# Performance work log

Hardware: AMD Instinct MI355X
Metric: run time of the kernel (lower is better)

## Reference

```python
import jax, jax.numpy as jnp
import numpy as np

V, E, H = 50000, 200, 256
B, R, S, W = 16, 16, 16, 32


def gru_last(x, Wih, Whh, bih, bhh):
    """PyTorch-style GRU, return final hidden state.
    x: [N, T, D]; Wih: [3H, D]; Whh: [3H, H]. Gate order: r, z, n."""
    gx = jnp.einsum('ntd,gd->ntg', x, Wih) + bih  # precompute input gates [N,T,3H]
    h0 = jnp.zeros((x.shape[0], Whh.shape[1]), x.dtype)

    def step(h, gxt):
        gh = h @ Whh.T + bhh
        xr, xz, xn = jnp.split(gxt, 3, axis=-1)
        hr, hz, hn = jnp.split(gh, 3, axis=-1)
        r = jax.nn.sigmoid(xr + hr)
        z = jax.nn.sigmoid(xz + hz)
        n = jnp.tanh(xn + r * hn)
        return (1.0 - z) * n + z * h, None

    h, _ = jax.lax.scan(step, h0, jnp.swapaxes(gx, 0, 1))
    return h  # [N, H]


def mlp(x, W1, b1, W2, b2):
    # Linear -> SELU -> (Dropout is identity in eval) -> Linear
    return jax.nn.selu(x @ W1.T + b1) @ W2.T + b2


def setup_inputs() -> dict:
    key = jax.random.key(0)
    ks = jax.random.split(key, 20)
    n = lambda k, shp: (jax.random.normal(k, shp, dtype=jnp.float32) * 0.05)
    inp = {
        'inputs': jax.random.randint(ks[0], (B, R, S, W), 0, V, dtype=jnp.int64),
        'emb': n(ks[1], (V, E)),
        'w_Wih': n(ks[2], (3 * H, E)), 'w_Whh': n(ks[3], (3 * H, H)),
        'w_bih': n(ks[4], (3 * H,)), 'w_bhh': n(ks[5], (3 * H,)),
        's_Wih': n(ks[6], (3 * H, H)), 's_Whh': n(ks[7], (3 * H, H)),
        's_bih': n(ks[8], (3 * H,)), 's_bhh': n(ks[9], (3 * H,)),
        'r_Wih': n(ks[10], (3 * H, H)), 'r_Whh': n(ks[11], (3 * H, H)),
        'r_bih': n(ks[12], (3 * H,)), 'r_bhh': n(ks[13], (3 * H,)),
        'rfc_W1': n(ks[14], (H // 2, H)), 'rfc_b1': n(ks[15], (H // 2,)),
        'rfc_W2': n(ks[16], (1, H // 2)), 'rfc_b2': jnp.zeros((1,), jnp.float32),
        'pfc_W1': n(ks[17], (H // 2, H)), 'pfc_b1': n(ks[18], (H // 2,)),
        'pfc_W2': n(ks[19], (1, H // 2)), 'pfc_b2': jnp.zeros((1,), jnp.float32),
    }
    return inp


def reference(inputs, emb, w_Wih, w_Whh, w_bih, w_bhh,
              s_Wih, s_Whh, s_bih, s_bhh,
              r_Wih, r_Whh, r_bih, r_bhh,
              rfc_W1, rfc_b1, rfc_W2, rfc_b2,
              pfc_W1, pfc_b1, pfc_W2, pfc_b2):
    b, r, s, w = inputs.shape
    x = emb[inputs]                                   # [B,R,S,W,E] (dropout = identity in eval)
    # word-level GRU over all sentences at once (batches the Python double loop)
    sent_h = gru_last(x.reshape(b * r * s, w, E), w_Wih, w_Whh, w_bih, w_bhh)  # [B*R*S, H]
    # sentence-level GRU per review
    rev_h = gru_last(sent_h.reshape(b * r, s, H), s_Wih, s_Whh, s_bih, s_bhh)  # [B*R, H]
    p_batch = rev_h.reshape(b, r, H)                  # [B, R, H]
    r_stars = mlp(p_batch, rfc_W1, rfc_b1, rfc_W2, rfc_b2)  # [B, R, 1]
    # review-level GRU per business
    biz_h = gru_last(p_batch, r_Wih, r_Whh, r_bih, r_bhh)   # [B, H]
    b_stars = mlp(biz_h, pfc_W1, pfc_b1, pfc_W2, pfc_b2)    # [B, 1]
    return (b_stars, r_stars)
```

## Files before the change

### kernel.cpp

```cpp
#include <hip/hip_runtime.h>
#include <math.h>

#define VOCAB 50000
#define EDIM  200
#define HDIM  256
#define G3    768
#define NSEQ1 4096
#define T1    32
#define NSEQ2 256
#define T2    16
#define NSEQ3 16
#define T3    16

using bf16x8 = __attribute__((ext_vector_type(8))) short;
using f32x4  = __attribute__((ext_vector_type(4))) float;

__device__ __forceinline__ float sigmoid_f(float x) {
    return 1.0f / (1.0f + __expf(-x));
}
__device__ __forceinline__ float tanh_f(float x) {
    return 1.0f - 2.0f / (__expf(2.0f * x) + 1.0f);
}
__device__ __forceinline__ short f2b(float f) {
    unsigned u = __float_as_uint(f);
    unsigned r = (u + 0x7fffu + ((u >> 16) & 1u)) >> 16;
    return (short)r;
}
__device__ __forceinline__ float b2f(unsigned short v) {
    return __uint_as_float((unsigned)v << 16);
}
__device__ __forceinline__ void lds_barrier() {
    asm volatile("s_waitcnt lgkmcnt(0)\n\ts_barrier" ::: "memory");
}

struct CvtJob { const float* src; short* dst; int kin; int kpad; };
struct CvtJobs { CvtJob j[6]; };

__global__ void convert6(CvtJobs jobs) {
    const CvtJob jb = jobs.j[blockIdx.y];
    const int r = blockIdx.x;
    for (int k = threadIdx.x; k < jb.kpad; k += blockDim.x)
        jb.dst[(size_t)r * jb.kpad + k] =
            (k < jb.kin) ? f2b(jb.src[(size_t)r * jb.kin + k]) : (short)0;
}

template <int KC, bool AF32, bool CBF16>
__global__ __launch_bounds__(512) void gemm_mfma(
    const void* __restrict__ Av, const short* __restrict__ WB,
    const float* __restrict__ bias, void* __restrict__ Cv,
    int M, int Keff) {
    constexpr int KPAD  = KC * 32;
    constexpr int CELLS = KPAD / 8;
    __shared__ short As[128 * 256];
    const int tid = threadIdx.x;
    const int m0 = blockIdx.x * 128;
    const int n0 = blockIdx.y * 192;

    {
        const int row  = tid >> 2;
        const int c0   = (tid & 3) * 8;
        const int rowg = m0 + row;
        const int vcell = Keff >> 3;
        for (int i = 0; i < 8; i++) {
            const int c = c0 + i;
            if (c >= CELLS) break;
            bf16x8 v;
            if (rowg < M && c < vcell) {
                if constexpr (AF32) {
                    const float* ap = (const float*)Av + (size_t)rowg * Keff + c * 8;
                    const float4 x = *(const float4*)ap;
                    const float4 y = *(const float4*)(ap + 4);
                    v[0] = f2b(x.x); v[1] = f2b(x.y); v[2] = f2b(x.z); v[3] = f2b(x.w);
                    v[4] = f2b(y.x); v[5] = f2b(y.y); v[6] = f2b(y.z); v[7] = f2b(y.w);
                } else {
                    const short* ap = (const short*)Av + (size_t)rowg * Keff + c * 8;
                    v = *(const bf16x8*)ap;
                }
            } else {
                v = (bf16x8)(short)0;
            }
            *(bf16x8*)&As[row * 256 + ((c ^ (row & 7)) << 3)] = v;
        }
    }
    __syncthreads();

    const int w  = tid >> 6;
    const int l  = tid & 63;
    const int lr = l & 15, lg = l >> 4;

    bf16x8 af[KC];
    {
        const int row = (w << 4) + lr;
#pragma unroll
        for (int kc = 0; kc < KC; kc++) {
            const int cell = kc * 4 + lg;
            af[kc] = *(const bf16x8*)&As[row * 256 + ((cell ^ (row & 7)) << 3)];
        }
    }
    f32x4 acc[12];
#pragma unroll
    for (int nt = 0; nt < 12; nt++) acc[nt] = (f32x4){0.f, 0.f, 0.f, 0.f};
#pragma unroll
    for (int nt = 0; nt < 12; nt++) {
        const short* wb = WB + (size_t)(n0 + nt * 16 + lr) * KPAD + lg * 8;
#pragma unroll
        for (int kc = 0; kc < KC; kc++) {
            bf16x8 bf = *(const bf16x8*)(wb + kc * 32);
            acc[nt] = __builtin_amdgcn_mfma_f32_16x16x32_bf16(af[kc], bf, acc[nt], 0, 0, 0);
        }
    }
#pragma unroll
    for (int nt = 0; nt < 12; nt++) {
        const int col = n0 + nt * 16 + lr;
        const float bv = bias[col];
#pragma unroll
        for (int q = 0; q < 4; q++) {
            const int row = m0 + (w << 4) + lg * 4 + q;
            if (row < M) {
                const float o = acc[nt][q] + bv;
                if constexpr (CBF16) ((short*)Cv)[(size_t)row * G3 + col] = f2b(o);
                else                 ((float*)Cv)[(size_t)row * G3 + col] = o;
            }
        }
    }
}

__global__ __launch_bounds__(1024) void gru_mfma(
    const int* __restrict__ idx,
    const short* __restrict__ gxb,
    const short* __restrict__ WB,
    const float* __restrict__ bhh,
    float* __restrict__ hf32,
    short* __restrict__ hb16,
    int T) {
    __shared__ short hsB[16 * 256];
    __shared__ int idxs[16 * T1];
    const int tid = threadIdx.x;
    const int n0 = blockIdx.x * 16;
    const int w  = tid >> 6, l = tid & 63;
    const int lr = l & 15, lg = l >> 4;
    const int jj = w * 16 + lr;

    for (int i = tid; i < 16 * 256; i += 1024) hsB[i] = 0;
    if (idx) {
        for (int i = tid; i < 16 * T; i += 1024) {
            const int s = i / T, p = i - s * T;
            int tk = idx[(size_t)(n0 + s) * T + p];
            idxs[s * T + p] = min(max(tk, 0), VOCAB - 1);
        }
    }

    const float bR = bhh[jj];
    const float bZ = bhh[256 + jj];
    const float bN = bhh[512 + jj];

    bf16x8 bw[3][8];
#pragma unroll
    for (int g = 0; g < 3; g++) {
        const short* wb = WB + (size_t)(g * 256 + jj) * 256 + lg * 8;
#pragma unroll
        for (int kc = 0; kc < 8; kc++)
            bw[g][kc] = *(const bf16x8*)(wb + kc * 32);
    }

    float hreg[4] = {0.f, 0.f, 0.f, 0.f};
    __syncthreads();

    unsigned short gA[12], gB[12];
    auto load_gx = [&](unsigned short (&buf)[12], int t) {
#pragma unroll
        for (int q = 0; q < 4; q++) {
            const int s = lg * 4 + q;
            size_t rowbase;
            if (idx) rowbase = (size_t)idxs[s * T + t] * G3;
            else     rowbase = ((size_t)(n0 + s) * T + t) * G3;
            const short* src = gxb + rowbase;
            buf[q * 3 + 0] = *(const unsigned short*)&src[jj];
            buf[q * 3 + 1] = *(const unsigned short*)&src[256 + jj];
            buf[q * 3 + 2] = *(const unsigned short*)&src[512 + jj];
        }
    };
    auto step = [&](const unsigned short (&buf)[12]) {
        bf16x8 af[8];
#pragma unroll
        for (int kc = 0; kc < 8; kc++) {
            const int cell = kc * 4 + lg;
            af[kc] = *(const bf16x8*)&hsB[lr * 256 + ((cell ^ (lr & 7)) << 3)];
        }
        lds_barrier();

        f32x4 acc[3];
#pragma unroll
        for (int g = 0; g < 3; g++) acc[g] = (f32x4){0.f, 0.f, 0.f, 0.f};
#pragma unroll
        for (int g = 0; g < 3; g++)
#pragma unroll
            for (int kc = 0; kc < 8; kc++)
                acc[g] = __builtin_amdgcn_mfma_f32_16x16x32_bf16(af[kc], bw[g][kc], acc[g], 0, 0, 0);

#pragma unroll
        for (int q = 0; q < 4; q++) {
            const int s = lg * 4 + q;
            const float xr = b2f(buf[q * 3 + 0]);
            const float xz = b2f(buf[q * 3 + 1]);
            const float xn = b2f(buf[q * 3 + 2]);
            const float r = sigmoid_f(xr + acc[0][q] + bR);
            const float z = sigmoid_f(xz + acc[1][q] + bZ);
            const float n = tanh_f(xn + r * (acc[2][q] + bN));
            const float h = (1.f - z) * n + z * hreg[q];
            hreg[q] = h;
            hsB[s * 256 + (((jj >> 3) ^ (s & 7)) << 3) + (jj & 7)] = f2b(h);
        }
        lds_barrier();
    };

    load_gx(gA, 0);
    for (int t = 0; t < T; t += 2) {
        if (t + 1 < T) load_gx(gB, t + 1);
        step(gA);
        if (t + 2 < T) load_gx(gA, t + 2);
        step(gB);
    }

#pragma unroll
    for (int q = 0; q < 4; q++) {
        const int s = lg * 4 + q;
        const size_t o = (size_t)(n0 + s) * HDIM + jj;
        if (hf32) hf32[o] = hreg[q];
        if (hb16) hb16[o] = f2b(hreg[q]);
    }
}

__global__ __launch_bounds__(128) void mlp_head(
    const float* __restrict__ hin, const float* __restrict__ W1,
    const float* __restrict__ b1, const float* __restrict__ W2,
    const float* __restrict__ b2, float* __restrict__ out) {
    const int row = blockIdx.x;
    const int gg = threadIdx.x;
    const float* h = hin + (size_t)row * HDIM;
    const float* wv1 = W1 + (size_t)gg * HDIM;
    float acc = 0.f;
#pragma unroll 4
    for (int k = 0; k < HDIM; k += 4) {
        const float4 hv = *(const float4*)&h[k];
        const float4 wv = *(const float4*)&wv1[k];
        acc += hv.x * wv.x; acc += hv.y * wv.y;
        acc += hv.z * wv.z; acc += hv.w * wv.w;
    }
    acc += b1[gg];
    const float alpha = 1.6732632423543772f;
    const float scale = 1.0507009873554805f;
    const float s = scale * (acc > 0.f ? acc : alpha * expm1f(acc));
    float v = s * W2[gg];

    __shared__ float red[128];
    red[gg] = v;
    __syncthreads();
    if (gg < 64) {
        float x = red[gg] + red[gg + 64];
#pragma unroll
        for (int off = 32; off; off >>= 1) x += __shfl_down(x, off);
        if (gg == 0) out[row] = x + b2[0];
    }
}

extern "C" void kernel_launch(void* const* d_in, const int* in_sizes, int n_in,
                              void* d_out, int out_size, void* d_ws, size_t ws_size,
                              hipStream_t stream) {
    const int*   idx    = (const int*)d_in[0];
    const float* emb    = (const float*)d_in[1];
    const float* w_Wih  = (const float*)d_in[2];
    const float* w_Whh  = (const float*)d_in[3];
    const float* w_bih  = (const float*)d_in[4];
    const float* w_bhh  = (const float*)d_in[5];
    const float* s_Wih  = (const float*)d_in[6];
    const float* s_Whh  = (const float*)d_in[7];
    const float* s_bih  = (const float*)d_in[8];
    const float* s_bhh  = (const float*)d_in[9];
    const float* r_Wih  = (const float*)d_in[10];
    const float* r_Whh  = (const float*)d_in[11];
    const float* r_bih  = (const float*)d_in[12];
    const float* r_bhh  = (const float*)d_in[13];
    const float* rfc_W1 = (const float*)d_in[14];
    const float* rfc_b1 = (const float*)d_in[15];
    const float* rfc_W2 = (const float*)d_in[16];
    const float* rfc_b2 = (const float*)d_in[17];
    const float* pfc_W1 = (const float*)d_in[18];
    const float* pfc_b1 = (const float*)d_in[19];
    const float* pfc_W2 = (const float*)d_in[20];
    const float* pfc_b2 = (const float*)d_in[21];

    float* out = (float*)d_out;

    short* sws = (short*)d_ws;
    short* Pb      = sws;
    short* gx2b    = Pb      + (size_t)VOCAB * G3;
    short* gx3b    = gx2b    + (size_t)NSEQ1 * G3;
    short* WhhB_w  = gx3b    + (size_t)NSEQ2 * G3;
    short* WihB_w  = WhhB_w  + (size_t)G3 * HDIM;
    short* sWihB   = WihB_w  + (size_t)G3 * 224;
    short* sWhhB   = sWihB   + (size_t)G3 * HDIM;
    short* rWihB   = sWhhB   + (size_t)G3 * HDIM;
    short* rWhhB   = rWihB   + (size_t)G3 * HDIM;
    short* sent_hB = rWhhB   + (size_t)G3 * HDIM;
    short* rev_hB  = sent_hB + (size_t)NSEQ1 * HDIM;
    float* fws     = (float*)(rev_hB + (size_t)NSEQ2 * HDIM);
    float* rev_h   = fws;
    float* biz_h   = rev_h + (size_t)NSEQ2 * HDIM;

    CvtJobs jobs;
    jobs.j[0] = {w_Whh, WhhB_w, HDIM, HDIM};
    jobs.j[1] = {w_Wih, WihB_w, EDIM, 224};
    jobs.j[2] = {s_Wih, sWihB, HDIM, HDIM};
    jobs.j[3] = {s_Whh, sWhhB, HDIM, HDIM};
    jobs.j[4] = {r_Wih, rWihB, HDIM, HDIM};
    jobs.j[5] = {r_Whh, rWhhB, HDIM, HDIM};
    convert6<<<dim3(G3, 6), 256, 0, stream>>>(jobs);

    gemm_mfma<7, true, true><<<dim3((VOCAB + 127) / 128, 4), 512, 0, stream>>>(
        emb, WihB_w, w_bih, Pb, VOCAB, EDIM);

    gru_mfma<<<NSEQ1 / 16, 1024, 0, stream>>>(
        idx, Pb, WhhB_w, w_bhh, nullptr, sent_hB, T1);

    gemm_mfma<8, false, true><<<dim3(NSEQ1 / 128, 4), 512, 0, stream>>>(
        sent_hB, sWihB, s_bih, gx2b, NSEQ1, HDIM);

    gru_mfma<<<NSEQ2 / 16, 1024, 0, stream>>>(
        nullptr, gx2b, sWhhB, s_bhh, rev_h, rev_hB, T2);

    mlp_head<<<NSEQ2, 128, 0, stream>>>(
        rev_h, rfc_W1, rfc_b1, rfc_W2, rfc_b2, out + 16);

    gemm_mfma<8, false, true><<<dim3(2, 4), 512, 0, stream>>>(
        rev_hB, rWihB, r_bih, gx3b, NSEQ2, HDIM);

    gru_mfma<<<1, 1024, 0, stream>>>(
        nullptr, gx3b, rWhhB, r_bhh, biz_h, nullptr, T3);

    mlp_head<<<NSEQ3, 128, 0, stream>>>(
        biz_h, pfc_W1, pfc_b1, pfc_W2, pfc_b2, out);
}
```

Before: 760.0 us.

## Halve GRU block to 512 threads, stage n-gate weights in LDS, 2 tiles per wave

The recurrent GRU kernel now runs with 512 threads per block instead of 1024, and each wave computes two 16-column tiles of the hidden state instead of one. The r and z gate weights stay in registers. The n-gate weight slice (256x256 bf16, 128 KB) moves into swizzled shared memory and is read inside the MFMA loop each step. The input-gate values are loaded packed as 32-bit pairs. The aim is to fit two blocks per CU with 512 threads each, and to interleave six independent MFMA chains per wave so MFMA latency is hidden better. In exchange, each step now does more LDS reads, and the large shared allocation may itself cap occupancy.

```diff
diff --git a/kernel.cpp b/kernel.cpp
--- a/kernel.cpp
+++ b/kernel.cpp
@@ -125,7 +125,7 @@
     }
 }
 
-__global__ __launch_bounds__(1024) void gru_mfma(
+__global__ __launch_bounds__(512, 2) void gru_mfma(
     const int* __restrict__ idx,
     const short* __restrict__ gxb,
     const short* __restrict__ WB,
@@ -133,83 +133,120 @@
     float* __restrict__ hf32,
     short* __restrict__ hb16,
     int T) {
+    __shared__ short wsN[256 * 256 / 2 * 2];
     __shared__ short hsB[16 * 256];
     __shared__ int idxs[16 * T1];
     const int tid = threadIdx.x;
     const int n0 = blockIdx.x * 16;
     const int w  = tid >> 6, l = tid & 63;
     const int lr = l & 15, lg = l >> 4;
-    const int jj = w * 16 + lr;
-
-    for (int i = tid; i < 16 * 256; i += 1024) hsB[i] = 0;
+    const int tt0 = w * 2;
+    const int jj0 = tt0 * 16 + lr;
+    const int jj1 = jj0 + 16;
+
+    for (int i = tid; i < 16 * 256; i += 512) hsB[i] = 0;
     if (idx) {
-        for (int i = tid; i < 16 * T; i += 1024) {
+        for (int i = tid; i < 16 * T; i += 512) {
             const int s = i / T, p = i - s * T;
             int tk = idx[(size_t)(n0 + s) * T + p];
             idxs[s * T + p] = min(max(tk, 0), VOCAB - 1);
         }
     }
-
-    const float bR = bhh[jj];
-    const float bZ = bhh[256 + jj];
-    const float bN = bhh[512 + jj];
-
-    bf16x8 bw[3][8];
-#pragma unroll
-    for (int g = 0; g < 3; g++) {
-        const short* wb = WB + (size_t)(g * 256 + jj) * 256 + lg * 8;
-#pragma unroll
-        for (int kc = 0; kc < 8; kc++)
-            bw[g][kc] = *(const bf16x8*)(wb + kc * 32);
-    }
-
-    float hreg[4] = {0.f, 0.f, 0.f, 0.f};
+#pragma unroll
+    for (int i = 0; i < 16; i++) {
+        const int cellidx = tid * 16 + i;
+        const int rr = cellidx >> 5;
+        const int cc = cellidx & 31;
+        bf16x8 v = *(const bf16x8*)&WB[(size_t)(512 + rr) * 256 + cc * 8];
+        *(bf16x8*)&wsN[rr * 256 + ((cc ^ (rr & 7)) << 3)] = v;
+    }
+
+    bf16x8 bwR[2][8], bwZ[2][8];
+#pragma unroll
+    for (int ti = 0; ti < 2; ti++) {
+        const int jjt = (tt0 + ti) * 16 + lr;
+#pragma unroll
+        for (int kc = 0; kc < 8; kc++) {
+            bwR[ti][kc] = *(const bf16x8*)&WB[(size_t)jjt * 256 + kc * 32 + lg * 8];
+            bwZ[ti][kc] = *(const bf16x8*)&WB[(size_t)(256 + jjt) * 256 + kc * 32 + lg * 8];
+        }
+    }
+    const float bR0 = bhh[jj0],       bR1 = bhh[jj1];
+    const float bZ0 = bhh[256 + jj0], bZ1 = bhh[256 + jj1];
+    const float bN0 = bhh[512 + jj0], bN1 = bhh[512 + jj1];
+
+    float hreg[2][4] = {};
     __syncthreads();
 
-    unsigned short gA[12], gB[12];
-    auto load_gx = [&](unsigned short (&buf)[12], int t) {
+    unsigned gA[12], gB[12];
+    auto load_gx = [&](unsigned (&buf)[12], int t) {
 #pragma unroll
         for (int q = 0; q < 4; q++) {
             const int s = lg * 4 + q;
             size_t rowbase;
             if (idx) rowbase = (size_t)idxs[s * T + t] * G3;
             else     rowbase = ((size_t)(n0 + s) * T + t) * G3;
-            const short* src = gxb + rowbase;
-            buf[q * 3 + 0] = *(const unsigned short*)&src[jj];
-            buf[q * 3 + 1] = *(const unsigned short*)&src[256 + jj];
-            buf[q * 3 + 2] = *(const unsigned short*)&src[512 + jj];
+            const unsigned short* src = (const unsigned short*)(gxb + rowbase);
+            const unsigned xr0 = src[jj0],       xr1 = src[jj1];
+            const unsigned xz0 = src[256 + jj0], xz1 = src[256 + jj1];
+            const unsigned xn0 = src[512 + jj0], xn1 = src[512 + jj1];
+            buf[q * 3 + 0] = xr0 | (xz0 << 16);
+            buf[q * 3 + 1] = xr1 | (xz1 << 16);
+            buf[q * 3 + 2] = xn0 | (xn1 << 16);
         }
     };
-    auto step = [&](const unsigned short (&buf)[12]) {
-        bf16x8 af[8];
+
+    auto step = [&](const unsigned (&buf)[12]) {
+        f32x4 aR[2], aZ[2], aN[2];
+#pragma unroll
+        for (int ti = 0; ti < 2; ti++) {
+            aR[ti] = (f32x4){0.f, 0.f, 0.f, 0.f};
+            aZ[ti] = (f32x4){0.f, 0.f, 0.f, 0.f};
+            aN[ti] = (f32x4){0.f, 0.f, 0.f, 0.f};
+        }
 #pragma unroll
         for (int kc = 0; kc < 8; kc++) {
             const int cell = kc * 4 + lg;
-            af[kc] = *(const bf16x8*)&hsB[lr * 256 + ((cell ^ (lr & 7)) << 3)];
+            const bf16x8 a  = *(const bf16x8*)&hsB[lr * 256 + ((cell ^ (lr & 7)) << 3)];
+            const bf16x8 n0f = *(const bf16x8*)&wsN[jj0 * 256 + ((cell ^ (jj0 & 7)) << 3)];
+            const bf16x8 n1f = *(const bf16x8*)&wsN[jj1 * 256 + ((cell ^ (jj1 & 7)) << 3)];
+            aR[0] = __builtin_amdgcn_mfma_f32_16x16x32_bf16(a, bwR[0][kc], aR[0], 0, 0, 0);
+            aZ[0] = __builtin_amdgcn_mfma_f32_16x16x32_bf16(a, bwZ[0][kc], aZ[0], 0, 0, 0);
+            aN[0] = __builtin_amdgcn_mfma_f32_16x16x32_bf16(a, n0f, aN[0], 0, 0, 0);
+            aR[1] = __builtin_amdgcn_mfma_f32_16x16x32_bf16(a, bwR[1][kc], aR[1], 0, 0, 0);
+            aZ[1] = __builtin_amdgcn_mfma_f32_16x16x32_bf16(a, bwZ[1][kc], aZ[1], 0, 0, 0);
+            aN[1] = __builtin_amdgcn_mfma_f32_16x16x32_bf16(a, n1f, aN[1], 0, 0, 0);
         }
         lds_barrier();
-
-        f32x4 acc[3];
-#pragma unroll
-        for (int g = 0; g < 3; g++) acc[g] = (f32x4){0.f, 0.f, 0.f, 0.f};
-#pragma unroll
-        for (int g = 0; g < 3; g++)
-#pragma unroll
-            for (int kc = 0; kc < 8; kc++)
-                acc[g] = __builtin_amdgcn_mfma_f32_16x16x32_bf16(af[kc], bw[g][kc], acc[g], 0, 0, 0);
 
 #pragma unroll
         for (int q = 0; q < 4; q++) {
             const int s = lg * 4 + q;
-            const float xr = b2f(buf[q * 3 + 0]);
-            const float xz = b2f(buf[q * 3 + 1]);
-            const float xn = b2f(buf[q * 3 + 2]);
-            const float r = sigmoid_f(xr + acc[0][q] + bR);
-            const float z = sigmoid_f(xz + acc[1][q] + bZ);
-            const float n = tanh_f(xn + r * (acc[2][q] + bN));
-            const float h = (1.f - z) * n + z * hreg[q];
-            hreg[q] = h;
-            hsB[s * 256 + (((jj >> 3) ^ (s & 7)) << 3) + (jj & 7)] = f2b(h);
+            const unsigned prz0 = buf[q * 3 + 0];
+            const unsigned prz1 = buf[q * 3 + 1];
+            const unsigned pn   = buf[q * 3 + 2];
+            {
+                const float xr = b2f((unsigned short)(prz0 & 0xffff));
+                const float xz = b2f((unsigned short)(prz0 >> 16));
+                const float xn = b2f((unsigned short)(pn & 0xffff));
+                const float r = sigmoid_f(xr + aR[0][q] + bR0);
+                const float z = sigmoid_f(xz + aZ[0][q] + bZ0);
+                const float n = tanh_f(xn + r * (aN[0][q] + bN0));
+                const float h = (1.f - z) * n + z * hreg[0][q];
+                hreg[0][q] = h;
+                hsB[s * 256 + (((jj0 >> 3) ^ (s & 7)) << 3) + (jj0 & 7)] = f2b(h);
+            }
+            {
+                const float xr = b2f((unsigned short)(prz1 & 0xffff));
+                const float xz = b2f((unsigned short)(prz1 >> 16));
+                const float xn = b2f((unsigned short)(pn >> 16));
+                const float r = sigmoid_f(xr + aR[1][q] + bR1);
+                const float z = sigmoid_f(xz + aZ[1][q] + bZ1);
+                const float n = tanh_f(xn + r * (aN[1][q] + bN1));
+                const float h = (1.f - z) * n + z * hreg[1][q];
+                hreg[1][q] = h;
+                hsB[s * 256 + (((jj1 >> 3) ^ (s & 7)) << 3) + (jj1 & 7)] = f2b(h);
+            }
         }
         lds_barrier();
     };
@@ -225,9 +262,10 @@
 #pragma unroll
     for (int q = 0; q < 4; q++) {
         const int s = lg * 4 + q;
-        const size_t o = (size_t)(n0 + s) * HDIM + jj;
-        if (hf32) hf32[o] = hreg[q];
-        if (hb16) hb16[o] = f2b(hreg[q]);
+        const size_t o0 = (size_t)(n0 + s) * HDIM + jj0;
+        const size_t o1 = (size_t)(n0 + s) * HDIM + jj1;
+        if (hf32) { hf32[o0] = hreg[0][q]; hf32[o1] = hreg[1][q]; }
+        if (hb16) { hb16[o0] = f2b(hreg[0][q]); hb16[o1] = f2b(hreg[1][q]); }
     }
 }
 
@@ -320,13 +358,13 @@
     gemm_mfma<7, true, true><<<dim3((VOCAB + 127) / 128, 4), 512, 0, stream>>>(
         emb, WihB_w, w_bih, Pb, VOCAB, EDIM);
 
-    gru_mfma<<<NSEQ1 / 16, 1024, 0, stream>>>(
+    gru_mfma<<<NSEQ1 / 16, 512, 0, stream>>>(
         idx, Pb, WhhB_w, w_bhh, nullptr, sent_hB, T1);
 
     gemm_mfma<8, false, true><<<dim3(NSEQ1 / 128, 4), 512, 0, stream>>>(
         sent_hB, sWihB, s_bih, gx2b, NSEQ1, HDIM);
 
-    gru_mfma<<<NSEQ2 / 16, 1024, 0, stream>>>(
+    gru_mfma<<<NSEQ2 / 16, 512, 0, stream>>>(
         nullptr, gx2b, sWhhB, s_bhh, rev_h, rev_hB, T2);
 
     mlp_head<<<NSEQ2, 128, 0, stream>>>(
@@ -335,7 +373,7 @@
     gemm_mfma<8, false, true><<<dim3(2, 4), 512, 0, stream>>>(
         rev_hB, rWihB, r_bih, gx3b, NSEQ2, HDIM);
 
-    gru_mfma<<<1, 1024, 0, stream>>>(
+    gru_mfma<<<1, 512, 0, stream>>>(
         nullptr, gx3b, rWhhB, r_bhh, biz_h, nullptr, T3);
 
     mlp_head<<<NSEQ3, 128, 0, stream>>>(
```

Result: faster. 626.8 us (-17.5%).
